# Kernel tuning notes

Hardware: AMD Instinct MI355X
Metric: run time of the kernel (lower is better)

## Reference

```python
import jax, jax.numpy as jnp
import numpy as np

B, T = 64, 512
V, E, H, L = 100000, 256, 256, 9


def _lstm(x, Wx, Wh, b):
    # x: [B,T,E] -> hs: [B,T,H]; Keras gate order i,f,c,o
    xg = jnp.einsum('bte,eg->btg', x, Wx) + b  # [B,T,4H]
    h0 = jnp.zeros((x.shape[0], Wh.shape[0]), x.dtype)

    def step(carry, xt):
        h, c = carry
        g = xt + h @ Wh
        i, f, gc, o = jnp.split(g, 4, axis=-1)
        c = jax.nn.sigmoid(f) * c + jax.nn.sigmoid(i) * jnp.tanh(gc)
        h = jax.nn.sigmoid(o) * jnp.tanh(c)
        return (h, c), h

    _, hs = jax.lax.scan(step, (h0, h0), jnp.swapaxes(xg, 0, 1))
    return jnp.swapaxes(hs, 0, 1)


def _crf_log_likelihood(logits, tags, seq_len, trans):
    # logits: [B,T,L], tags: [B,T] int, seq_len: [B] int, trans: [L,L]
    Bb, Tt, Ll = logits.shape
    t_idx = jnp.arange(Tt)
    mask = (t_idx[None, :] < seq_len[:, None]).astype(logits.dtype)  # [B,T]
    # gold path score: unary + pairwise transitions
    unary = jnp.take_along_axis(logits, tags[..., None], axis=-1)[..., 0]  # [B,T]
    unary_score = jnp.sum(unary * mask, axis=-1)
    binary = trans[tags[:, :-1], tags[:, 1:]]  # [B,T-1]
    binary_score = jnp.sum(binary * mask[:, 1:], axis=-1)
    score = unary_score + binary_score
    # forward algorithm (log partition)
    alpha0 = logits[:, 0]  # [B,L]
    step_mask = t_idx[1:, None] < seq_len[None, :]  # [T-1,B]

    def step(alpha, xs):
        logit_t, m = xs  # [B,L], [B]
        new = jax.nn.logsumexp(alpha[:, :, None] + trans[None], axis=1) + logit_t
        alpha = jnp.where(m[:, None], new, alpha)
        return alpha, None

    alpha, _ = jax.lax.scan(step, alpha0, (jnp.swapaxes(logits[:, 1:], 0, 1), step_mask))
    log_norm = jax.nn.logsumexp(alpha, axis=-1)  # [B]
    return score - log_norm


def setup_inputs() -> dict:
    key = jax.random.key(0)
    ks = jax.random.split(key, 12)
    s = 0.05
    return {
        'tokens': jax.random.randint(ks[0], (B, T), 0, V),
        'labels': jax.random.randint(ks[1], (B, T), 0, L),
        'emb_table': jax.random.normal(ks[2], (V, E), jnp.float32) * s,
        'Wx_f': jax.random.normal(ks[3], (E, 4 * H), jnp.float32) * s,
        'Wh_f': jax.random.normal(ks[4], (H, 4 * H), jnp.float32) * s,
        'b_f': jnp.zeros((4 * H,), jnp.float32),
        'Wx_b': jax.random.normal(ks[5], (E, 4 * H), jnp.float32) * s,
        'Wh_b': jax.random.normal(ks[6], (H, 4 * H), jnp.float32) * s,
        'b_b': jnp.zeros((4 * H,), jnp.float32),
        'W_dense': jax.random.normal(ks[7], (2 * H, L), jnp.float32) * s,
        'b_dense': jnp.zeros((L,), jnp.float32),
        'trans': jax.random.uniform(ks[8], (L, L), jnp.float32),
    }


def reference(tokens, labels, emb_table, Wx_f, Wh_f, b_f, Wx_b, Wh_b, b_b, W_dense, b_dense, trans):
    # seq_len = count of non-pad (nonzero) tokens, as in the original call()
    seq_len = jnp.sum((tokens != 0).astype(jnp.int32), axis=-1)  # [B]
    emb = emb_table[tokens]  # [B,T,E]  (dropout inactive at inference)
    h_fwd = _lstm(emb, Wx_f, Wh_f, b_f)
    h_bwd = _lstm(emb[:, ::-1], Wx_b, Wh_b, b_b)[:, ::-1]
    enc = jnp.concatenate([h_fwd, h_bwd], axis=-1)  # [B,T,2H]
    logits = enc @ W_dense + b_dense  # [B,T,L]
    ll = _crf_log_likelihood(logits, labels, seq_len, trans)  # [B]
    return logits, seq_len, ll
```

## Files before the change

kernel.cpp:

```cpp
#include <hip/hip_runtime.h>
#include <hip/hip_fp16.h>


typedef unsigned int  uint32;
typedef unsigned short ushort16;
typedef unsigned long long uint64;
typedef __attribute__((ext_vector_type(8))) short  short8;
typedef __attribute__((ext_vector_type(4))) float  floatx4;
typedef __attribute__((ext_vector_type(2))) _Float16 half2t;

#define BB 64
#define TT 512
#define NT (BB*TT)
#define G4 1024
#define NL 9

__device__ inline float bf2f(ushort16 u) {
  return __builtin_bit_cast(float, ((uint32)u) << 16);
}
__device__ inline ushort16 f2bf(float f) {
  uint32 u = __builtin_bit_cast(uint32, f);
  u += 0x7fffu + ((u >> 16) & 1u);
  return (ushort16)(u >> 16);
}
__device__ inline float sigf(float x)  { return 1.0f / (1.0f + __expf(-x)); }
__device__ inline float tanhf_(float x){ return 1.0f - 2.0f / (1.0f + __expf(2.0f * x)); }

__device__ inline float fdot2_(uint32 w, half2t h, float acc) {
  return __builtin_amdgcn_fdot2(__builtin_bit_cast(half2t, w), h, acc, false);
}

__global__ __launch_bounds__(64) void k_seqlen(const int* __restrict__ tokens,
                                               int* __restrict__ slen,
                                               float* __restrict__ out_sl) {
  const int b = blockIdx.x, lane = threadIdx.x;
  int cnt = 0;
  for (int t = lane; t < TT; t += 64) cnt += (tokens[b * TT + t] != 0) ? 1 : 0;
  #pragma unroll
  for (int off = 32; off >= 1; off >>= 1) cnt += __shfl_down(cnt, off, 64);
  if (lane == 0) { slen[b] = cnt; out_sl[b] = (float)cnt; }
}

__global__ __launch_bounds__(256) void k_embed(const int* __restrict__ tokens,
                                               const float* __restrict__ emb,
                                               ushort16* __restrict__ A) {
  const int f = blockIdx.x * 256 + threadIdx.x;
  const int e = f * 4;
  const int row = e >> 8;
  const int col = e & 255;
  const int tok = tokens[row];
  const float4 v = *(const float4*)(emb + (size_t)tok * 256 + col);
  uint32 lo = (uint32)f2bf(v.x) | ((uint32)f2bf(v.y) << 16);
  uint32 hi = (uint32)f2bf(v.z) | ((uint32)f2bf(v.w) << 16);
  *(uint2*)(A + e) = make_uint2(lo, hi);
}

__global__ __launch_bounds__(256) void k_wxprep(const float* __restrict__ Wxf,
                                                const float* __restrict__ Wxb,
                                                ushort16* __restrict__ BT) {
  const int id = blockIdx.x * 256 + threadIdx.x;
  const int c = id >> 8, k = id & 255;
  const float v = (c < G4) ? Wxf[k * G4 + c] : Wxb[k * G4 + (c - G4)];
  BT[c * 256 + k] = f2bf(v);
}

__global__ __launch_bounds__(256) void k_whprep(const float* __restrict__ Wh,
                                                uint32* __restrict__ W2) {
  const int id = blockIdx.x * 256 + threadIdx.x;
  const int k2 = id >> 10, c = id & 1023;
  const float w0 = Wh[(2 * k2) * G4 + c];
  const float w1 = Wh[(2 * k2 + 1) * G4 + c];
  const ushort16 b0 = __builtin_bit_cast(ushort16, (_Float16)w0);
  const ushort16 b1 = __builtin_bit_cast(ushort16, (_Float16)w1);
  W2[id] = ((uint32)b1 << 16) | (uint32)b0;
}

__global__ __launch_bounds__(256) void k_gemm_xg(const ushort16* __restrict__ A,
                                                 const ushort16* __restrict__ BT,
                                                 const float* __restrict__ bias_f,
                                                 const float* __restrict__ bias_b,
                                                 ushort16* __restrict__ xgf,
                                                 ushort16* __restrict__ xgb) {
  __shared__ __align__(16) ushort16 As[64 * 36];
  __shared__ __align__(16) ushort16 Bs[64 * 36];
  const int m0 = blockIdx.x * 64;
  const int n0 = blockIdx.y * 64;
  const int tid = threadIdx.x;
  const int wave = tid >> 6, lane = tid & 63;
  const int lr = tid >> 2;
  const int lc = (tid & 3) * 8;
  const int am = lane & 15, aq = lane >> 4;
  floatx4 acc[4];
  #pragma unroll
  for (int j = 0; j < 4; ++j) acc[j] = (floatx4){0.f, 0.f, 0.f, 0.f};

  for (int k0 = 0; k0 < 256; k0 += 32) {
    const uint4 va = *(const uint4*)(A  + ((m0 + lr) * 256 + k0 + lc));
    const uint4 vb = *(const uint4*)(BT + ((n0 + lr) * 256 + k0 + lc));
    *(uint2*)&As[lr * 36 + lc]     = make_uint2(va.x, va.y);
    *(uint2*)&As[lr * 36 + lc + 4] = make_uint2(va.z, va.w);
    *(uint2*)&Bs[lr * 36 + lc]     = make_uint2(vb.x, vb.y);
    *(uint2*)&Bs[lr * 36 + lc + 4] = make_uint2(vb.z, vb.w);
    __syncthreads();
    union { uint2 u[2]; short8 s; } fa, fb;
    fa.u[0] = *(const uint2*)&As[(wave * 16 + am) * 36 + aq * 8];
    fa.u[1] = *(const uint2*)&As[(wave * 16 + am) * 36 + aq * 8 + 4];
    #pragma unroll
    for (int j = 0; j < 4; ++j) {
      fb.u[0] = *(const uint2*)&Bs[(j * 16 + am) * 36 + aq * 8];
      fb.u[1] = *(const uint2*)&Bs[(j * 16 + am) * 36 + aq * 8 + 4];
      acc[j] = __builtin_amdgcn_mfma_f32_16x16x32_bf16(fa.s, fb.s, acc[j], 0, 0, 0);
    }
    __syncthreads();
  }
  const int orow = m0 + wave * 16 + aq * 4;
  #pragma unroll
  for (int j = 0; j < 4; ++j) {
    const int col = n0 + j * 16 + am;
    const float bv = (col < G4) ? bias_f[col] : bias_b[col - G4];
    #pragma unroll
    for (int r = 0; r < 4; ++r) {
      const float v = acc[j][r] + bv;
      const int row = orow + r;
      if (col < G4) xgf[row * G4 + col] = f2bf(v);
      else          xgb[row * G4 + (col - G4)] = f2bf(v);
    }
  }
}

__global__ __launch_bounds__(256) void k_zero(uint64* __restrict__ xh) {
  xh[blockIdx.x * 256 + threadIdx.x] = 0ull;
}

__global__ __launch_bounds__(512, 2) void k_lstm(const ushort16* __restrict__ xgf,
                                                 const ushort16* __restrict__ xgb,
                                                 const uint32* __restrict__ Whf,
                                                 const uint32* __restrict__ Whb,
                                                 uint64* __restrict__ xh,
                                                 float* __restrict__ enc) {
  __shared__ __align__(16) uint32 h2[2][128];
  __shared__ float gl[512];
  const int bid  = blockIdx.x;
  const int dir  = bid >> 7;
  const int b    = (bid >> 1) & 63;
  const int half = bid & 1;
  const int tid  = threadIdx.x;
  const int w = tid >> 6, l = tid & 63;
  const int q = tid >> 7, r = tid & 127;
  const int col = q * 256 + half * 128 + r;
  const ushort16* __restrict__ xg = dir ? xgb : xgf;
  const uint32* __restrict__ W2   = dir ? Whb : Whf;
  uint64* const xmine = xh + ((size_t)bid << 7);
  const uint64* const xpeer = xh + ((size_t)(bid ^ 1) << 7);

  const int ownBase  = half * 64;
  const int peerBase = 64 - ownBase;
  uint32 wv[128];
  #pragma unroll
  for (int i = 0; i < 64; ++i) wv[i]      = W2[(ownBase  + i) * 1024 + col];
  #pragma unroll
  for (int i = 0; i < 64; ++i) wv[64 + i] = W2[(peerBase + i) * 1024 + col];
  #pragma unroll
  for (int i = 0; i < 128; ++i) asm volatile("" : "+v"(wv[i]));

  if (tid < 128) { h2[0][tid] = 0u; }
  float c_state = 0.f;
  __syncthreads();

  const int t0 = dir ? (TT - 1) : 0;
  ushort16 xA = xg[(size_t)(b * TT + t0) * G4 + col];

#define HC(u) __builtin_bit_cast(half2t, u)
#define LD8(B) { t0_=hb[(B)+0]; t1_=hb[(B)+1]; t2_=hb[(B)+2]; t3_=hb[(B)+3]; \
                 t4_=hb[(B)+4]; t5_=hb[(B)+5]; t6_=hb[(B)+6]; t7_=hb[(B)+7]; }
#define GR4(T,K) { a0 = fdot2_(wv[(K)+0], HC(T.x), a0); \
                   a1 = fdot2_(wv[(K)+1], HC(T.y), a1); \
                   a2 = fdot2_(wv[(K)+2], HC(T.z), a2); \
                   a3 = fdot2_(wv[(K)+3], HC(T.w), a3); }
#define C8(KB) { GR4(t0_,(KB)+0) GR4(t1_,(KB)+4)  GR4(t2_,(KB)+8)  GR4(t3_,(KB)+12) \
                 GR4(t4_,(KB)+16) GR4(t5_,(KB)+20) GR4(t6_,(KB)+24) GR4(t7_,(KB)+28) }

  for (int s = 0; s < TT; ++s) {
    const int par = s & 1;
    float a0 = bf2f(xA), a1 = 0.f, a2 = 0.f, a3 = 0.f;
    if (s + 1 < TT) {
      const int t1 = dir ? (TT - 2 - s) : (s + 1);
      xA = xg[(size_t)(b * TT + t1) * G4 + col];
    }
    const uint4* hb = (const uint4*)h2[par];
    uint4 t0_, t1_, t2_, t3_, t4_, t5_, t6_, t7_;
    LD8(0)  C8(0)
    LD8(8)  C8(32)
    if (w == 0 && s > 0) {
      const uint32 want = (uint32)s;
      uint64 v;
      for (;;) {
        v = __hip_atomic_load(xpeer + (par << 6) + l,
                              __ATOMIC_RELAXED, __HIP_MEMORY_SCOPE_AGENT);
        if (__all((uint32)(v >> 32) == want)) break;
        __builtin_amdgcn_s_sleep(1);
      }
      h2[par][64 + l] = (uint32)v;
    }
    __syncthreads();
    LD8(16) C8(64)
    LD8(24) C8(96)
    gl[tid] = (a0 + a1) + (a2 + a3);
    __syncthreads();
    if (tid < 128) {
      const float gi = gl[tid];
      const float gf = gl[128 + tid];
      const float gg = gl[256 + tid];
      const float go = gl[384 + tid];
      c_state = sigf(gf) * c_state + sigf(gi) * tanhf_(gg);
      const float h = sigf(go) * tanhf_(c_state);
      const int hv = (int)(uint32)__builtin_bit_cast(ushort16, (_Float16)h);
      const int ho = __shfl_xor(hv, 1, 64);
      if (!(tid & 1)) {
        const uint32 pk = ((uint32)hv & 0xffffu) | ((uint32)ho << 16);
        if (s + 1 < TT) {
          const uint64 pv = ((uint64)(uint32)(s + 1) << 32) | (uint64)pk;
          __hip_atomic_store(xmine + ((par ^ 1) << 6) + (tid >> 1), pv,
                             __ATOMIC_RELAXED, __HIP_MEMORY_SCOPE_AGENT);
        }
        h2[par ^ 1][tid >> 1] = pk;
      }
      const int t = dir ? (TT - 1 - s) : s;
      enc[(size_t)(b * TT + t) * 512 + dir * 256 + half * 128 + tid] = h;
    }
    __syncthreads();
  }
#undef HC
#undef LD8
#undef GR4
#undef C8
}

__global__ __launch_bounds__(256) void k_dense(const float* __restrict__ enc,
                                               const float* __restrict__ Wd,
                                               const float* __restrict__ bd,
                                               float* __restrict__ logits) {
  __shared__ float Wl[512 * NL];
  __shared__ float bl[NL];
  const int tid = threadIdx.x;
  for (int i = tid; i < 512 * NL; i += 256) Wl[i] = Wd[i];
  if (tid < NL) bl[tid] = bd[tid];
  __syncthreads();
  const int wave = tid >> 6, lane = tid & 63;
  const int row = blockIdx.x * 4 + wave;
  const float* er = enc + (size_t)row * 512;
  float p[NL];
  #pragma unroll
  for (int c = 0; c < NL; ++c) p[c] = 0.f;
  #pragma unroll
  for (int u = 0; u < 8; ++u) {
    const int k = u * 64 + lane;
    const float v = er[k];
    const float* wr = &Wl[k * NL];
    #pragma unroll
    for (int c = 0; c < NL; ++c) p[c] += v * wr[c];
  }
  #pragma unroll
  for (int c = 0; c < NL; ++c) {
    #pragma unroll
    for (int off = 32; off >= 1; off >>= 1) p[c] += __shfl_down(p[c], off, 64);
  }
  if (lane == 0) {
    float* orow = logits + (size_t)row * NL;
    #pragma unroll
    for (int c = 0; c < NL; ++c) orow[c] = p[c] + bl[c];
  }
}

__global__ __launch_bounds__(64) void k_crf(const float* __restrict__ logits,
                                            const int* __restrict__ labels,
                                            const int* __restrict__ slen,
                                            const float* __restrict__ trans,
                                            float* __restrict__ out_ll) {
  __shared__ float tr[NL * NL];
  __shared__ float alpha[NL];
  const int b = blockIdx.x;
  const int lane = threadIdx.x;
  for (int i = lane; i < NL * NL; i += 64) tr[i] = trans[i];
  __syncthreads();
  const int len = slen[b];
  const int* tg = labels + b * TT;
  const float* lg = logits + (size_t)b * TT * NL;
  float s = 0.f;
  for (int t = lane; t < TT; t += 64)
    if (t < len) s += lg[t * NL + tg[t]];
  for (int t = lane; t < TT - 1; t += 64)
    if (t + 1 < len) s += tr[tg[t] * NL + tg[t + 1]];
  #pragma unroll
  for (int off = 32; off >= 1; off >>= 1) s += __shfl_down(s, off, 64);
  if (lane < NL) alpha[lane] = lg[lane];
  __syncthreads();
  if (lane < NL) {
    const int j = lane;
    for (int t = 1; t < TT; ++t) {
      if (t < len) {
        float av[NL];
        float m = -1e30f;
        #pragma unroll
        for (int i = 0; i < NL; ++i) { av[i] = alpha[i] + tr[i * NL + j]; m = fmaxf(m, av[i]); }
        float ss = 0.f;
        #pragma unroll
        for (int i = 0; i < NL; ++i) ss += __expf(av[i] - m);
        const float nj = m + __logf(ss) + lg[t * NL + j];
        alpha[j] = nj;
      }
    }
  }
  __syncthreads();
  if (lane == 0) {
    float m = -1e30f;
    #pragma unroll
    for (int i = 0; i < NL; ++i) m = fmaxf(m, alpha[i]);
    float ss = 0.f;
    #pragma unroll
    for (int i = 0; i < NL; ++i) ss += __expf(alpha[i] - m);
    out_ll[b] = s - (m + __logf(ss));
  }
}

extern "C" void kernel_launch(void* const* d_in, const int* in_sizes, int n_in,
                              void* d_out, int out_size, void* d_ws, size_t ws_size,
                              hipStream_t stream) {
  (void)in_sizes; (void)n_in; (void)out_size; (void)ws_size;
  const int*   tokens = (const int*)d_in[0];
  const int*   labels = (const int*)d_in[1];
  const float* emb    = (const float*)d_in[2];
  const float* Wxf    = (const float*)d_in[3];
  const float* Whf    = (const float*)d_in[4];
  const float* bf_    = (const float*)d_in[5];
  const float* Wxb    = (const float*)d_in[6];
  const float* Whb    = (const float*)d_in[7];
  const float* bb_    = (const float*)d_in[8];
  const float* Wd     = (const float*)d_in[9];
  const float* bd     = (const float*)d_in[10];
  const float* trans  = (const float*)d_in[11];
  float* out = (float*)d_out;

  char* ws = (char*)d_ws;
  ushort16* A    = (ushort16*)(ws + 0);
  ushort16* BT   = (ushort16*)(ws + 16777216);
  uint32*   W2f  = (uint32*)  (ws + 17825792);
  uint32*   W2b  = (uint32*)  (ws + 18350080);
  ushort16* xgf  = (ushort16*)(ws + 18874368);
  ushort16* xgb  = (ushort16*)(ws + 85983232);
  float*    enc  = (float*)   (ws + 153092096);
  int*      slen = (int*)     (ws + 220200960);
  uint64*   xh   = (uint64*)  (ws + 0);

  k_seqlen<<<BB, 64, 0, stream>>>(tokens, slen, out + NT * NL);
  k_embed <<<NT * 256 / 4 / 256, 256, 0, stream>>>(tokens, emb, A);
  k_wxprep<<<2048 * 256 / 256, 256, 0, stream>>>(Wxf, Wxb, BT);
  k_whprep<<<128 * 1024 / 256, 256, 0, stream>>>(Whf, W2f);
  k_whprep<<<128 * 1024 / 256, 256, 0, stream>>>(Whb, W2b);
  k_gemm_xg<<<dim3(NT / 64, 2048 / 64), 256, 0, stream>>>(A, BT, bf_, bb_, xgf, xgb);
  k_zero  <<<128, 256, 0, stream>>>(xh);
  k_lstm  <<<256, 512, 0, stream>>>(xgf, xgb, W2f, W2b, xh, enc);
  k_dense <<<NT / 4, 256, 0, stream>>>(enc, Wd, bd, out);
  k_crf   <<<BB, 64, 0, stream>>>(out, labels, slen, trans, out + NT * NL + BB);
}
```

Before: 1.346 ms.

## Use LDS-only barriers, spread gate activations across all threads in LSTM step

```diff
diff --git a/kernel.cpp b/kernel.cpp
--- a/kernel.cpp
+++ b/kernel.cpp
@@ -28,6 +28,13 @@
 
 __device__ inline float fdot2_(uint32 w, half2t h, float acc) {
   return __builtin_amdgcn_fdot2(__builtin_bit_cast(half2t, w), h, acc, false);
+}
+
+__device__ inline void bar_lds() {
+  __builtin_amdgcn_sched_barrier(0);
+  asm volatile("s_waitcnt lgkmcnt(0)" ::: "memory");
+  __builtin_amdgcn_s_barrier();
+  __builtin_amdgcn_sched_barrier(0);
 }
 
 __global__ __launch_bounds__(64) void k_seqlen(const int* __restrict__ tokens,
@@ -171,14 +178,11 @@
   ushort16 xA = xg[(size_t)(b * TT + t0) * G4 + col];
 
 #define HC(u) __builtin_bit_cast(half2t, u)
-#define LD8(B) { t0_=hb[(B)+0]; t1_=hb[(B)+1]; t2_=hb[(B)+2]; t3_=hb[(B)+3]; \
-                 t4_=hb[(B)+4]; t5_=hb[(B)+5]; t6_=hb[(B)+6]; t7_=hb[(B)+7]; }
-#define GR4(T,K) { a0 = fdot2_(wv[(K)+0], HC(T.x), a0); \
-                   a1 = fdot2_(wv[(K)+1], HC(T.y), a1); \
-                   a2 = fdot2_(wv[(K)+2], HC(T.z), a2); \
-                   a3 = fdot2_(wv[(K)+3], HC(T.w), a3); }
-#define C8(KB) { GR4(t0_,(KB)+0) GR4(t1_,(KB)+4)  GR4(t2_,(KB)+8)  GR4(t3_,(KB)+12) \
-                 GR4(t4_,(KB)+16) GR4(t5_,(KB)+20) GR4(t6_,(KB)+24) GR4(t7_,(KB)+28) }
+#define GR4(B) { const uint4 hq = hb[B]; \
+                 a0 = fdot2_(wv[(B)*4+0], HC(hq.x), a0); \
+                 a1 = fdot2_(wv[(B)*4+1], HC(hq.y), a1); \
+                 a2 = fdot2_(wv[(B)*4+2], HC(hq.z), a2); \
+                 a3 = fdot2_(wv[(B)*4+3], HC(hq.w), a3); }
 
   for (int s = 0; s < TT; ++s) {
     const int par = s & 1;
@@ -188,9 +192,8 @@
       xA = xg[(size_t)(b * TT + t1) * G4 + col];
     }
     const uint4* hb = (const uint4*)h2[par];
-    uint4 t0_, t1_, t2_, t3_, t4_, t5_, t6_, t7_;
-    LD8(0)  C8(0)
-    LD8(8)  C8(32)
+    GR4(0)  GR4(1)  GR4(2)  GR4(3)  GR4(4)  GR4(5)  GR4(6)  GR4(7)
+    GR4(8)  GR4(9)  GR4(10) GR4(11) GR4(12) GR4(13) GR4(14) GR4(15)
     if (w == 0 && s > 0) {
       const uint32 want = (uint32)s;
       uint64 v;
@@ -202,18 +205,22 @@
       }
       h2[par][64 + l] = (uint32)v;
     }
-    __syncthreads();
-    LD8(16) C8(64)
-    LD8(24) C8(96)
-    gl[tid] = (a0 + a1) + (a2 + a3);
-    __syncthreads();
+    bar_lds();
+    GR4(16) GR4(17) GR4(18) GR4(19) GR4(20) GR4(21) GR4(22) GR4(23)
+    GR4(24) GR4(25) GR4(26) GR4(27) GR4(28) GR4(29) GR4(30) GR4(31)
+    {
+      float tv = (a0 + a1) + (a2 + a3);
+      tv = (q == 2) ? tanhf_(tv) : sigf(tv);
+      gl[tid] = tv;
+    }
+    bar_lds();
     if (tid < 128) {
-      const float gi = gl[tid];
-      const float gf = gl[128 + tid];
-      const float gg = gl[256 + tid];
-      const float go = gl[384 + tid];
-      c_state = sigf(gf) * c_state + sigf(gi) * tanhf_(gg);
-      const float h = sigf(go) * tanhf_(c_state);
+      const float I = gl[tid];
+      const float F = gl[128 + tid];
+      const float G = gl[256 + tid];
+      const float O = gl[384 + tid];
+      c_state = F * c_state + I * G;
+      const float h = O * tanhf_(c_state);
       const int hv = (int)(uint32)__builtin_bit_cast(ushort16, (_Float16)h);
       const int ho = __shfl_xor(hv, 1, 64);
       if (!(tid & 1)) {
@@ -228,12 +235,10 @@
       const int t = dir ? (TT - 1 - s) : s;
       enc[(size_t)(b * TT + t) * 512 + dir * 256 + half * 128 + tid] = h;
     }
-    __syncthreads();
+    bar_lds();
   }
 #undef HC
-#undef LD8
 #undef GR4
-#undef C8
 }
 
 __global__ __launch_bounds__(256) void k_dense(const float* __restrict__ enc,
```

Result: faster. 1.302 ms (-3.3%).
